# Optimization experiments

Measured on AMD Instinct MI355X. Metric: run time of the kernel, lower is better.

Reference implementation:

```python
import jax, jax.numpy as jnp
import numpy as np

D_MODEL = 1024
N_HEADS = 16
D_K = D_MODEL // N_HEADS


def setup_inputs() -> dict:
    key = jax.random.key(0)
    ks = jax.random.split(key, 10)
    B, L = 2, 2048
    s = 1.0 / np.sqrt(D_MODEL)
    inp = {
        "x": jax.random.normal(ks[0], (B, L, D_MODEL), dtype=jnp.float32),
        "bond_influence": jax.random.uniform(ks[1], (B, L, L), dtype=jnp.float32),
        "Wq": jax.random.uniform(ks[2], (D_MODEL, D_MODEL), jnp.float32, -s, s),
        "bq": jax.random.uniform(ks[3], (D_MODEL,), jnp.float32, -s, s),
        "Wk": jax.random.uniform(ks[4], (D_MODEL, D_MODEL), jnp.float32, -s, s),
        "bk": jax.random.uniform(ks[5], (D_MODEL,), jnp.float32, -s, s),
        "Wv": jax.random.uniform(ks[6], (D_MODEL, D_MODEL), jnp.float32, -s, s),
        "bv": jax.random.uniform(ks[7], (D_MODEL,), jnp.float32, -s, s),
        "Wo": jax.random.uniform(ks[8], (D_MODEL, D_MODEL), jnp.float32, -s, s),
        "bo": jax.random.uniform(ks[9], (D_MODEL,), jnp.float32, -s, s),
    }
    return inp


def reference(x, bond_influence, Wq, bq, Wk, bk, Wv, bv, Wo, bo):
    B, L, _ = x.shape
    # QKV projections -> [B, H, L, d_k]
    def proj(W, b):
        return (x @ W + b).reshape(B, L, N_HEADS, D_K).transpose(0, 2, 1, 3)
    Q = proj(Wq, bq)
    K = proj(Wk, bk)
    V = proj(Wv, bv)
    # scores: [B, H, L, L], scaled then modulated by per-batch bond influence
    scores = jnp.einsum('bhqd,bhkd->bhqk', Q, K) / jnp.sqrt(jnp.float32(D_K))
    scores = scores * bond_influence[:, None, :, :]
    attn = jax.nn.softmax(scores, axis=-1)
    out = jnp.einsum('bhqk,bhkd->bhqd', attn, V)  # [B, H, L, d_k]
    out = out.transpose(0, 2, 1, 3).reshape(B, L, D_MODEL)
    return out @ Wo + bo
```

## Files before the change

kernel.cpp:

```cpp
#include <hip/hip_runtime.h>
#include <stdint.h>

typedef unsigned short u16;
typedef __attribute__((ext_vector_type(8))) short bf16x8;
typedef __attribute__((ext_vector_type(4))) float f32x4;

__device__ __forceinline__ u16 f2bf(float f) {
    union { float f; uint32_t u; } v; v.f = f;
    uint32_t u = v.u + 0x7fffu + ((v.u >> 16) & 1u);
    return (u16)(u >> 16);
}

__device__ __forceinline__ uint32_t cvtpk(float a, float b) {
    uint32_t d;
    asm("v_cvt_pk_bf16_f32 %0, %1, %2" : "=v"(d) : "v"(a), "v"(b));
    return d;
}

__device__ __forceinline__ void gld16(const void* g, void* l) {
    __builtin_amdgcn_global_load_lds((const __attribute__((address_space(1))) void*)g,
                                     (__attribute__((address_space(3))) void*)l,
                                     16, 0, 0);
}

__device__ __forceinline__ void plswap16(uint32_t& a, uint32_t& b) {
    asm volatile("v_permlane16_swap_b32 %0, %1" : "+v"(a), "+v"(b));
}


__global__ void cvt_bf16_kernel(const float* __restrict__ s, u16* __restrict__ d, int n4) {
    int i = blockIdx.x * blockDim.x + threadIdx.x;
    const int stride = gridDim.x * blockDim.x;
    for (; i < n4; i += stride) {
        float4 v = ((const float4*)s)[i];
        ushort4 o;
        o.x = f2bf(v.x); o.y = f2bf(v.y); o.z = f2bf(v.z); o.w = f2bf(v.w);
        ((ushort4*)d)[i] = o;
    }
}

__global__ void transpose4_bf16_kernel(const float* __restrict__ Wq, const float* __restrict__ Wk,
                                       const float* __restrict__ Wv, const float* __restrict__ Wo,
                                       u16* __restrict__ dqkv, u16* __restrict__ dо) {
    __shared__ float tile[32][33];
    const int z = blockIdx.z;
    const float* src = (z == 0) ? Wq : (z == 1) ? Wk : (z == 2) ? Wv : Wo;
    u16* dst = (z < 3) ? (dqkv + (size_t)z * 1024 * 1024) : dо;
    const int tx = threadIdx.x, ty = threadIdx.y;
    const int bx = blockIdx.x * 32, by = blockIdx.y * 32;
#pragma unroll
    for (int i = ty; i < 32; i += 8)
        tile[i][tx] = src[(size_t)(by + i) * 1024 + bx + tx];
    __syncthreads();
#pragma unroll
    for (int i = ty; i < 32; i += 8)
        dst[(size_t)(bx + i) * 1024 + by + tx] = f2bf(tile[tx][i]);
}


template <int EPI>
__global__ __launch_bounds__(256) void gemm128(
    const u16* __restrict__ A, const u16* __restrict__ Bt,
    const float* __restrict__ bias0, const float* __restrict__ bias1,
    const float* __restrict__ bias2,
    u16* __restrict__ o_q, u16* __restrict__ o_k, u16* __restrict__ o_vt,
    float* __restrict__ o_f)
{
    constexpr int K = 1024;
    __shared__ u16 As[128 * 32];
    __shared__ u16 Bs[128 * 32];
    const int t = threadIdx.x;
    const int lane = t & 63, w = t >> 6;
    const int wm = w >> 1, wn = w & 1;
    const int g = lane >> 4, r = lane & 15;
    const int mbase = blockIdx.y * 128, nbase = blockIdx.x * 128;

    const f32x4 zero4 = {0.f, 0.f, 0.f, 0.f};
    f32x4 acc[4][4];
#pragma unroll
    for (int m = 0; m < 4; ++m)
#pragma unroll
        for (int n = 0; n < 4; ++n) acc[m][n] = zero4;

    for (int k0 = 0; k0 < K; k0 += 32) {
#pragma unroll
        for (int i = 0; i < 2; ++i) {
            const int base = i * 256 + (w << 6);
            const int idx = base + lane;
            const int row = idx >> 2, cc = (idx & 3) << 3;
            gld16(A + (size_t)(mbase + row) * K + k0 + cc, (char*)As + base * 16);
            gld16(Bt + (size_t)(nbase + row) * K + k0 + cc, (char*)Bs + base * 16);
        }
        __syncthreads();

        bf16x8 af[4], bfr[4];
#pragma unroll
        for (int m = 0; m < 4; ++m)
            af[m] = *(const bf16x8*)&As[(wm * 64 + m * 16 + r) * 32 + g * 8];
#pragma unroll
        for (int n = 0; n < 4; ++n)
            bfr[n] = *(const bf16x8*)&Bs[(wn * 64 + n * 16 + r) * 32 + g * 8];
        __builtin_amdgcn_s_setprio(1);
#pragma unroll
        for (int m = 0; m < 4; ++m)
#pragma unroll
            for (int n = 0; n < 4; ++n)
                acc[m][n] = __builtin_amdgcn_mfma_f32_16x16x32_bf16(af[m], bfr[n], acc[m][n], 0, 0, 0);
        __builtin_amdgcn_s_setprio(0);
        __syncthreads();
    }

#pragma unroll
    for (int m = 0; m < 4; ++m) {
#pragma unroll
        for (int n = 0; n < 4; ++n) {
            const int c = nbase + wn * 64 + n * 16 + r;
#pragma unroll
            for (int j = 0; j < 4; ++j) {
                const int rr = mbase + wm * 64 + m * 16 + g * 4 + j;
                const float y = acc[m][n][j];
                if (EPI == 0) {
                    const int which = c >> 10, d = c & 1023;
                    const int b = rr >> 11, l = rr & 2047;
                    const int h = d >> 6, dd = d & 63;
                    const size_t bh = (size_t)(b * 16 + h);
                    if (which == 0) {
                        o_q[(bh * 2048 + l) * 64 + dd] = f2bf((y + bias0[d]) * 0.125f);
                    } else if (which == 1) {
                        o_k[(bh * 2048 + l) * 64 + dd] = f2bf(y + bias1[d]);
                    } else {
                        o_vt[(bh * 64 + dd) * 2048 + l] = f2bf(y + bias2[d]);
                    }
                } else {
                    o_f[(size_t)rr * 1024 + c] = y + bias0[c];
                }
            }
        }
    }
}


#define ATTN_STEP(CUR, BD, BDN, PREF)                                                        \
    {                                                                                        \
        if (PREF) {                                                                          \
            const int ktn = kt + 32;                                                         \
            _Pragma("unroll")                                                                \
            for (int i = 0; i < 2; ++i) {                                                    \
                const int idx = i * 128 + t;                                                 \
                const int row = idx >> 3, ch = idx & 7;                                      \
                gld16(kb + kvBase + (size_t)(ktn + row) * 64 + ((ch ^ (row & 7)) << 3),      \
                      (char*)&Ks[CUR ^ 1][0] + idx * 16);                                    \
            }                                                                                \
            _Pragma("unroll")                                                                \
            for (int i = 0; i < 2; ++i) {                                                    \
                const int idx = i * 128 + t;                                                 \
                const int row = idx >> 2, ch = idx & 3;                                      \
                const int chs = ch ^ ((row & 3) ^ ((row >> 2) & 3));                         \
                gld16(vtb + vtBase + (size_t)row * 2048 + ktn + (chs << 3),                  \
                      (char*)&Vs[CUR ^ 1][0] + idx * 16);                                    \
            }                                                                                \
            BDN[0] = *(const float4*)&bondf[bondRowG + ktn];                                 \
            BDN[1] = *(const float4*)&bondf[bondRowG + ktn + 16];                            \
        }                                                                                    \
        bf16x8 k00, k01, k10, k11;                                                           \
        k00 = *(const bf16x8*)((const char*)&Ks[CUR][0] + (r) * 128 + ((g ^ sw) * 16));      \
        k01 = *(const bf16x8*)((const char*)&Ks[CUR][0] + (16 + r) * 128 + ((g ^ sw) * 16)); \
        k10 = *(const bf16x8*)((const char*)&Ks[CUR][0] + (r) * 128 + (((4 + g) ^ sw) * 16)); \
        k11 = *(const bf16x8*)((const char*)&Ks[CUR][0] + (16 + r) * 128 + (((4 + g) ^ sw) * 16)); \
        f32x4 st0, st1;                                                                      \
        __builtin_amdgcn_s_setprio(1);                                                       \
        st0 = __builtin_amdgcn_mfma_f32_16x16x32_bf16(k00, aq0, zero4, 0, 0, 0);             \
        st1 = __builtin_amdgcn_mfma_f32_16x16x32_bf16(k01, aq0, zero4, 0, 0, 0);             \
        st0 = __builtin_amdgcn_mfma_f32_16x16x32_bf16(k10, aq1, st0, 0, 0, 0);               \
        st1 = __builtin_amdgcn_mfma_f32_16x16x32_bf16(k11, aq1, st1, 0, 0, 0);               \
        __builtin_amdgcn_s_setprio(0);                                                       \
        const float p0 = __expf(st0[0] * BD[0].x);                                           \
        const float p1 = __expf(st0[1] * BD[0].y);                                           \
        const float p2 = __expf(st0[2] * BD[0].z);                                           \
        const float p3 = __expf(st0[3] * BD[0].w);                                           \
        const float p4 = __expf(st1[0] * BD[1].x);                                           \
        const float p5 = __expf(st1[1] * BD[1].y);                                           \
        const float p6 = __expf(st1[2] * BD[1].z);                                           \
        const float p7 = __expf(st1[3] * BD[1].w);                                           \
        sm += ((p0 + p1) + (p2 + p3)) + ((p4 + p5) + (p6 + p7));                             \
        uint32_t l0 = cvtpk(p0, p1), h0 = cvtpk(p2, p3);                                     \
        uint32_t l1 = cvtpk(p4, p5), h1 = cvtpk(p6, p7);                                     \
        plswap16(l0, l1);                                                                    \
        plswap16(h0, h1);                                                                    \
        union { uint32_t u[4]; bf16x8 v; } ap_;                                              \
        ap_.u[0] = l0; ap_.u[1] = h0; ap_.u[2] = l1; ap_.u[3] = h1;                          \
        bf16x8 bv0, bv1, bv2, bv3;                                                           \
        bv0 = *(const bf16x8*)((const char*)&Vs[CUR][0] + (r) * 64 + ((pg ^ sv) * 16));      \
        bv1 = *(const bf16x8*)((const char*)&Vs[CUR][0] + (16 + r) * 64 + ((pg ^ sv) * 16)); \
        bv2 = *(const bf16x8*)((const char*)&Vs[CUR][0] + (32 + r) * 64 + ((pg ^ sv) * 16)); \
        bv3 = *(const bf16x8*)((const char*)&Vs[CUR][0] + (48 + r) * 64 + ((pg ^ sv) * 16)); \
        __builtin_amdgcn_s_setprio(1);                                                       \
        o0 = __builtin_amdgcn_mfma_f32_16x16x32_bf16(ap_.v, bv0, o0, 0, 0, 0);               \
        o1 = __builtin_amdgcn_mfma_f32_16x16x32_bf16(ap_.v, bv1, o1, 0, 0, 0);               \
        o2 = __builtin_amdgcn_mfma_f32_16x16x32_bf16(ap_.v, bv2, o2, 0, 0, 0);               \
        o3 = __builtin_amdgcn_mfma_f32_16x16x32_bf16(ap_.v, bv3, o3, 0, 0, 0);               \
        __builtin_amdgcn_s_setprio(0);                                                       \
        __syncthreads();                                                                     \
        kt += 32;                                                                            \
    }

__global__ __launch_bounds__(128, 4) void attn_kernel(
    const u16* __restrict__ qb, const u16* __restrict__ kb,
    const u16* __restrict__ vtb, const float* __restrict__ bondf,
    u16* __restrict__ attnout)
{
    __shared__ u16 Ks[2][32 * 64];
    __shared__ u16 Vs[2][64 * 32];
    const int t = threadIdx.x;
    const int lane = t & 63, w = t >> 6;
    const int g = lane >> 4, r = lane & 15;
    const int sw = r & 7;
    const int sv = (r & 3) ^ ((r >> 2) & 3);
    const int pg = ((g & 1) << 1) | (g >> 1);
    const int flat = blockIdx.x;
    const int wg = (flat & 7) * 256 + (flat >> 3);
    const int bh = wg >> 6, qt = wg & 63;
    const int b = bh >> 4, h = bh & 15;
    const int q0 = qt * 32 + w * 16;
    const size_t kvBase = (size_t)bh * 2048 * 64;
    const size_t vtBase = (size_t)bh * 64 * 2048;
    const size_t bondRowG = ((size_t)b * 2048 + q0 + r) * 2048 + g * 4;

    const bf16x8 aq0 = *(const bf16x8*)&qb[kvBase + (size_t)(q0 + r) * 64 + g * 8];
    const bf16x8 aq1 = *(const bf16x8*)&qb[kvBase + (size_t)(q0 + r) * 64 + 32 + g * 8];

    const f32x4 zero4 = {0.f, 0.f, 0.f, 0.f};
    f32x4 o0 = zero4, o1 = zero4, o2 = zero4, o3 = zero4;
    float sm = 0.f;

#pragma unroll
    for (int i = 0; i < 2; ++i) {
        const int idx = i * 128 + t;
        const int row = idx >> 3, ch = idx & 7;
        gld16(kb + kvBase + (size_t)row * 64 + ((ch ^ (row & 7)) << 3),
              (char*)&Ks[0][0] + idx * 16);
    }
#pragma unroll
    for (int i = 0; i < 2; ++i) {
        const int idx = i * 128 + t;
        const int row = idx >> 2, ch = idx & 3;
        const int chs = ch ^ ((row & 3) ^ ((row >> 2) & 3));
        gld16(vtb + vtBase + (size_t)row * 2048 + (chs << 3),
              (char*)&Vs[0][0] + idx * 16);
    }
    float4 bdA[2], bdB[2];
    bdA[0] = *(const float4*)&bondf[bondRowG];
    bdA[1] = *(const float4*)&bondf[bondRowG + 16];
    __syncthreads();

    int kt = 0;
    for (int s = 0; s < 32; ++s) {
        ATTN_STEP(0, bdA, bdB, true)
        ATTN_STEP(1, bdB, bdA, (s < 31))
    }

    sm += __shfl_xor(sm, 16, 64);
    sm += __shfl_xor(sm, 32, 64);
#pragma unroll
    for (int j = 0; j < 4; ++j) {
        const float inv = 1.f / __shfl(sm, g * 4 + j, 16);
        const size_t orow = ((size_t)b * 2048 + q0 + g * 4 + j) * 1024 + h * 64;
        attnout[orow + r]      = f2bf(o0[j] * inv);
        attnout[orow + 16 + r] = f2bf(o1[j] * inv);
        attnout[orow + 32 + r] = f2bf(o2[j] * inv);
        attnout[orow + 48 + r] = f2bf(o3[j] * inv);
    }
}


extern "C" void kernel_launch(void* const* d_in, const int* in_sizes, int n_in,
                              void* d_out, int out_size, void* d_ws, size_t ws_size,
                              hipStream_t stream) {
    (void)in_sizes; (void)n_in; (void)out_size; (void)ws_size;
    const float* x    = (const float*)d_in[0];
    const float* bond = (const float*)d_in[1];
    const float* Wq   = (const float*)d_in[2];
    const float* bq   = (const float*)d_in[3];
    const float* Wk   = (const float*)d_in[4];
    const float* bk   = (const float*)d_in[5];
    const float* Wv   = (const float*)d_in[6];
    const float* bv   = (const float*)d_in[7];
    const float* Wo   = (const float*)d_in[8];
    const float* bo   = (const float*)d_in[9];
    float* out = (float*)d_out;

    char* ws = (char*)d_ws;
    u16* xb      = (u16*)(ws);
    u16* wqkvt   = (u16*)(ws + 8388608);
    u16* wot     = (u16*)(ws + 14680064);
    u16* qb      = (u16*)(ws + 16777216);
    u16* kb_     = (u16*)(ws + 25165824);
    u16* vtb     = (u16*)(ws + 33554432);
    u16* attnout = (u16*)(ws + 58720256);

    dim3 tb(32, 8);
    transpose4_bf16_kernel<<<dim3(32, 32, 4), tb, 0, stream>>>(Wq, Wk, Wv, Wo, wqkvt, wot);
    cvt_bf16_kernel<<<1024, 256, 0, stream>>>(x, xb, 4194304 / 4);

    gemm128<0><<<dim3(24, 32), 256, 0, stream>>>(xb, wqkvt, bq, bk, bv, qb, kb_, vtb, nullptr);
    attn_kernel<<<dim3(2048), 128, 0, stream>>>(qb, kb_, vtb, bond, attnout);
    gemm128<1><<<dim3(8, 32), 256, 0, stream>>>(attnout, wot, bo, nullptr, nullptr,
                                                nullptr, nullptr, nullptr, out);
}
```

Measured before the change: 188.3 us.

## Use single-wave attention blocks handling 32 query rows with exp2 and vmcnt waits

The attention kernel now runs one 64-lane wave per block covering 32 query rows (two 16-row fragments), so each K/V tile in LDS is reused across twice as many queries and the per-step __syncthreads is replaced by an explicit s_waitcnt vmcnt. The Q scale folds in log2(e) so the softmax uses the raw v_exp_f32 (exp2) instruction instead of __expf. This cuts barrier overhead and LDS/global traffic per query but doubles register use per wave, which may lower occupancy. A scale parameter was also added to the conversion kernel but is set to 1.

```diff
diff --git a/kernel.cpp b/kernel.cpp
--- a/kernel.cpp
+++ b/kernel.cpp
@@ -10,7 +10,11 @@
     uint32_t u = v.u + 0x7fffu + ((v.u >> 16) & 1u);
     return (u16)(u >> 16);
 }
-
+__device__ __forceinline__ float vexp2(float x) {
+    float d;
+    asm("v_exp_f32 %0, %1" : "=v"(d) : "v"(x));
+    return d;
+}
 __device__ __forceinline__ uint32_t cvtpk(float a, float b) {
     uint32_t d;
     asm("v_cvt_pk_bf16_f32 %0, %1, %2" : "=v"(d) : "v"(a), "v"(b));
@@ -28,13 +32,15 @@
 }
 
 
-__global__ void cvt_bf16_kernel(const float* __restrict__ s, u16* __restrict__ d, int n4) {
+__global__ void cvt_bf16_kernel(const float* __restrict__ s, u16* __restrict__ d, int n4,
+                                float scale) {
     int i = blockIdx.x * blockDim.x + threadIdx.x;
     const int stride = gridDim.x * blockDim.x;
     for (; i < n4; i += stride) {
         float4 v = ((const float4*)s)[i];
         ushort4 o;
-        o.x = f2bf(v.x); o.y = f2bf(v.y); o.z = f2bf(v.z); o.w = f2bf(v.w);
+        o.x = f2bf(v.x * scale); o.y = f2bf(v.y * scale);
+        o.z = f2bf(v.z * scale); o.w = f2bf(v.w * scale);
         ((ushort4*)d)[i] = o;
     }
 }
@@ -125,7 +131,7 @@
                     const int h = d >> 6, dd = d & 63;
                     const size_t bh = (size_t)(b * 16 + h);
                     if (which == 0) {
-                        o_q[(bh * 2048 + l) * 64 + dd] = f2bf((y + bias0[d]) * 0.125f);
+                        o_q[(bh * 2048 + l) * 64 + dd] = f2bf((y + bias0[d]) * 0.18033688011112042f);
                     } else if (which == 1) {
                         o_k[(bh * 2048 + l) * 64 + dd] = f2bf(y + bias1[d]);
                     } else {
@@ -140,79 +146,98 @@
 }
 
 
-#define ATTN_STEP(CUR, BD, BDN, PREF)                                                        \
+#define ATTN_STEP(CUR, BD, BDN, PREF, WAITN)                                                 \
     {                                                                                        \
         if (PREF) {                                                                          \
-            const int ktn = kt + 32;                                                         \
-            _Pragma("unroll")                                                                \
-            for (int i = 0; i < 2; ++i) {                                                    \
-                const int idx = i * 128 + t;                                                 \
+            const int kt2 = kt + 32;                                                         \
+            _Pragma("unroll")                                                                \
+            for (int i = 0; i < 4; ++i) {                                                    \
+                const int idx = i * 64 + lane;                                               \
                 const int row = idx >> 3, ch = idx & 7;                                      \
-                gld16(kb + kvBase + (size_t)(ktn + row) * 64 + ((ch ^ (row & 7)) << 3),      \
+                gld16(kb + kvBase + (size_t)(kt2 + row) * 64 + ((ch ^ (row & 7)) << 3),      \
                       (char*)&Ks[CUR ^ 1][0] + idx * 16);                                    \
             }                                                                                \
             _Pragma("unroll")                                                                \
-            for (int i = 0; i < 2; ++i) {                                                    \
-                const int idx = i * 128 + t;                                                 \
+            for (int i = 0; i < 4; ++i) {                                                    \
+                const int idx = i * 64 + lane;                                               \
                 const int row = idx >> 2, ch = idx & 3;                                      \
                 const int chs = ch ^ ((row & 3) ^ ((row >> 2) & 3));                         \
-                gld16(vtb + vtBase + (size_t)row * 2048 + ktn + (chs << 3),                  \
+                gld16(vtb + vtBase + (size_t)row * 2048 + kt2 + (chs << 3),                  \
                       (char*)&Vs[CUR ^ 1][0] + idx * 16);                                    \
             }                                                                                \
-            BDN[0] = *(const float4*)&bondf[bondRowG + ktn];                                 \
-            BDN[1] = *(const float4*)&bondf[bondRowG + ktn + 16];                            \
+            BDN[0] = *(const float4*)&bondf[bondRow0 + kt2 + g * 4];                         \
+            BDN[1] = *(const float4*)&bondf[bondRow0 + kt2 + 16 + g * 4];                    \
+            BDN[2] = *(const float4*)&bondf[bondRow0 + 32768 + kt2 + g * 4];                 \
+            BDN[3] = *(const float4*)&bondf[bondRow0 + 32768 + kt2 + 16 + g * 4];            \
         }                                                                                    \
-        bf16x8 k00, k01, k10, k11;                                                           \
-        k00 = *(const bf16x8*)((const char*)&Ks[CUR][0] + (r) * 128 + ((g ^ sw) * 16));      \
-        k01 = *(const bf16x8*)((const char*)&Ks[CUR][0] + (16 + r) * 128 + ((g ^ sw) * 16)); \
-        k10 = *(const bf16x8*)((const char*)&Ks[CUR][0] + (r) * 128 + (((4 + g) ^ sw) * 16)); \
-        k11 = *(const bf16x8*)((const char*)&Ks[CUR][0] + (16 + r) * 128 + (((4 + g) ^ sw) * 16)); \
-        f32x4 st0, st1;                                                                      \
+        asm volatile("s_waitcnt vmcnt(" #WAITN ")" ::: "memory");                            \
+        __builtin_amdgcn_sched_barrier(0);                                                   \
+                                                \
+        bf16x8 kfr[2][2];                                                                    \
+        _Pragma("unroll")                                                                    \
+        for (int kz = 0; kz < 2; ++kz)                                                       \
+            _Pragma("unroll")                                                                \
+            for (int kf = 0; kf < 2; ++kf)                                                   \
+                kfr[kz][kf] = *(const bf16x8*)((const char*)&Ks[CUR][0] +                    \
+                                (kf * 16 + r) * 128 + (((kz * 4 + g) ^ sw) * 16));           \
+        f32x4 st[2][2];                                                                      \
         __builtin_amdgcn_s_setprio(1);                                                       \
-        st0 = __builtin_amdgcn_mfma_f32_16x16x32_bf16(k00, aq0, zero4, 0, 0, 0);             \
-        st1 = __builtin_amdgcn_mfma_f32_16x16x32_bf16(k01, aq0, zero4, 0, 0, 0);             \
-        st0 = __builtin_amdgcn_mfma_f32_16x16x32_bf16(k10, aq1, st0, 0, 0, 0);               \
-        st1 = __builtin_amdgcn_mfma_f32_16x16x32_bf16(k11, aq1, st1, 0, 0, 0);               \
+        _Pragma("unroll")                                                                    \
+        for (int qf = 0; qf < 2; ++qf)                                                       \
+            _Pragma("unroll")                                                                \
+            for (int kf = 0; kf < 2; ++kf) {                                                 \
+                st[qf][kf] = __builtin_amdgcn_mfma_f32_16x16x32_bf16(                        \
+                    kfr[0][kf], aq[qf][0], zero4, 0, 0, 0);                                  \
+                st[qf][kf] = __builtin_amdgcn_mfma_f32_16x16x32_bf16(                        \
+                    kfr[1][kf], aq[qf][1], st[qf][kf], 0, 0, 0);                             \
+            }                                                                                \
         __builtin_amdgcn_s_setprio(0);                                                       \
-        const float p0 = __expf(st0[0] * BD[0].x);                                           \
-        const float p1 = __expf(st0[1] * BD[0].y);                                           \
-        const float p2 = __expf(st0[2] * BD[0].z);                                           \
-        const float p3 = __expf(st0[3] * BD[0].w);                                           \
-        const float p4 = __expf(st1[0] * BD[1].x);                                           \
-        const float p5 = __expf(st1[1] * BD[1].y);                                           \
-        const float p6 = __expf(st1[2] * BD[1].z);                                           \
-        const float p7 = __expf(st1[3] * BD[1].w);                                           \
-        sm += ((p0 + p1) + (p2 + p3)) + ((p4 + p5) + (p6 + p7));                             \
-        uint32_t l0 = cvtpk(p0, p1), h0 = cvtpk(p2, p3);                                     \
-        uint32_t l1 = cvtpk(p4, p5), h1 = cvtpk(p6, p7);                                     \
-        plswap16(l0, l1);                                                                    \
-        plswap16(h0, h1);                                                                    \
-        union { uint32_t u[4]; bf16x8 v; } ap_;                                              \
-        ap_.u[0] = l0; ap_.u[1] = h0; ap_.u[2] = l1; ap_.u[3] = h1;                          \
-        bf16x8 bv0, bv1, bv2, bv3;                                                           \
-        bv0 = *(const bf16x8*)((const char*)&Vs[CUR][0] + (r) * 64 + ((pg ^ sv) * 16));      \
-        bv1 = *(const bf16x8*)((const char*)&Vs[CUR][0] + (16 + r) * 64 + ((pg ^ sv) * 16)); \
-        bv2 = *(const bf16x8*)((const char*)&Vs[CUR][0] + (32 + r) * 64 + ((pg ^ sv) * 16)); \
-        bv3 = *(const bf16x8*)((const char*)&Vs[CUR][0] + (48 + r) * 64 + ((pg ^ sv) * 16)); \
+                                                \
+        bf16x8 ap[2];                                                                        \
+        _Pragma("unroll")                                                                    \
+        for (int qf = 0; qf < 2; ++qf) {                                                     \
+            const float p0 = vexp2(st[qf][0][0] * BD[2 * qf].x);                             \
+            const float p1 = vexp2(st[qf][0][1] * BD[2 * qf].y);                             \
+            const float p2 = vexp2(st[qf][0][2] * BD[2 * qf].z);                             \
+            const float p3 = vexp2(st[qf][0][3] * BD[2 * qf].w);                             \
+            const float p4 = vexp2(st[qf][1][0] * BD[2 * qf + 1].x);                         \
+            const float p5 = vexp2(st[qf][1][1] * BD[2 * qf + 1].y);                         \
+            const float p6 = vexp2(st[qf][1][2] * BD[2 * qf + 1].z);                         \
+            const float p7 = vexp2(st[qf][1][3] * BD[2 * qf + 1].w);                         \
+            sm[qf] += ((p0 + p1) + (p2 + p3)) + ((p4 + p5) + (p6 + p7));                     \
+            uint32_t l0 = cvtpk(p0, p1), h0 = cvtpk(p2, p3);                                 \
+            uint32_t l1 = cvtpk(p4, p5), h1 = cvtpk(p6, p7);                                 \
+            plswap16(l0, l1);                                                                \
+            plswap16(h0, h1);                                                                \
+            union { uint32_t u[4]; bf16x8 v; } a_;                                           \
+            a_.u[0] = l0; a_.u[1] = h0; a_.u[2] = l1; a_.u[3] = h1;                          \
+            ap[qf] = a_.v;                                                                   \
+        }                                                                                    \
+                                              \
+        bf16x8 bv_[4];                                                                       \
+        _Pragma("unroll")                                                                    \
+        for (int nf = 0; nf < 4; ++nf)                                                       \
+            bv_[nf] = *(const bf16x8*)((const char*)&Vs[CUR][0] +                            \
+                        (nf * 16 + r) * 64 + ((pg ^ sv) << 4));                              \
         __builtin_amdgcn_s_setprio(1);                                                       \
-        o0 = __builtin_amdgcn_mfma_f32_16x16x32_bf16(ap_.v, bv0, o0, 0, 0, 0);               \
-        o1 = __builtin_amdgcn_mfma_f32_16x16x32_bf16(ap_.v, bv1, o1, 0, 0, 0);               \
-        o2 = __builtin_amdgcn_mfma_f32_16x16x32_bf16(ap_.v, bv2, o2, 0, 0, 0);               \
-        o3 = __builtin_amdgcn_mfma_f32_16x16x32_bf16(ap_.v, bv3, o3, 0, 0, 0);               \
+        _Pragma("unroll")                                                                    \
+        for (int qf = 0; qf < 2; ++qf)                                                       \
+            _Pragma("unroll")                                                                \
+            for (int nf = 0; nf < 4; ++nf)                                                   \
+                o[qf][nf] = __builtin_amdgcn_mfma_f32_16x16x32_bf16(                         \
+                    ap[qf], bv_[nf], o[qf][nf], 0, 0, 0);                                    \
         __builtin_amdgcn_s_setprio(0);                                                       \
-        __syncthreads();                                                                     \
         kt += 32;                                                                            \
     }
 
-__global__ __launch_bounds__(128, 4) void attn_kernel(
+__global__ __launch_bounds__(64) void attn_kernel(
     const u16* __restrict__ qb, const u16* __restrict__ kb,
     const u16* __restrict__ vtb, const float* __restrict__ bondf,
     u16* __restrict__ attnout)
 {
     __shared__ u16 Ks[2][32 * 64];
     __shared__ u16 Vs[2][64 * 32];
-    const int t = threadIdx.x;
-    const int lane = t & 63, w = t >> 6;
+    const int lane = threadIdx.x & 63;
     const int g = lane >> 4, r = lane & 15;
     const int sw = r & 7;
     const int sv = (r & 3) ^ ((r >> 2) & 3);
@@ -221,55 +246,70 @@
     const int wg = (flat & 7) * 256 + (flat >> 3);
     const int bh = wg >> 6, qt = wg & 63;
     const int b = bh >> 4, h = bh & 15;
-    const int q0 = qt * 32 + w * 16;
+    const int q0 = qt * 32;
     const size_t kvBase = (size_t)bh * 2048 * 64;
     const size_t vtBase = (size_t)bh * 64 * 2048;
-    const size_t bondRowG = ((size_t)b * 2048 + q0 + r) * 2048 + g * 4;
-
-    const bf16x8 aq0 = *(const bf16x8*)&qb[kvBase + (size_t)(q0 + r) * 64 + g * 8];
-    const bf16x8 aq1 = *(const bf16x8*)&qb[kvBase + (size_t)(q0 + r) * 64 + 32 + g * 8];
+    const size_t bondRow0 = ((size_t)b * 2048 + q0 + r) * 2048;
+
+    bf16x8 aq[2][2];
+#pragma unroll
+    for (int qf = 0; qf < 2; ++qf)
+#pragma unroll
+        for (int kz = 0; kz < 2; ++kz)
+            aq[qf][kz] = *(const bf16x8*)&qb[kvBase + (size_t)(q0 + qf * 16 + r) * 64 + kz * 32 + g * 8];
 
     const f32x4 zero4 = {0.f, 0.f, 0.f, 0.f};
-    f32x4 o0 = zero4, o1 = zero4, o2 = zero4, o3 = zero4;
-    float sm = 0.f;
-
-#pragma unroll
-    for (int i = 0; i < 2; ++i) {
-        const int idx = i * 128 + t;
+    f32x4 o[2][4];
+#pragma unroll
+    for (int qf = 0; qf < 2; ++qf)
+#pragma unroll
+        for (int nf = 0; nf < 4; ++nf) o[qf][nf] = zero4;
+    float sm[2] = {0.f, 0.f};
+
+#pragma unroll
+    for (int i = 0; i < 4; ++i) {
+        const int idx = i * 64 + lane;
         const int row = idx >> 3, ch = idx & 7;
         gld16(kb + kvBase + (size_t)row * 64 + ((ch ^ (row & 7)) << 3),
               (char*)&Ks[0][0] + idx * 16);
     }
 #pragma unroll
-    for (int i = 0; i < 2; ++i) {
-        const int idx = i * 128 + t;
+    for (int i = 0; i < 4; ++i) {
+        const int idx = i * 64 + lane;
         const int row = idx >> 2, ch = idx & 3;
         const int chs = ch ^ ((row & 3) ^ ((row >> 2) & 3));
         gld16(vtb + vtBase + (size_t)row * 2048 + (chs << 3),
               (char*)&Vs[0][0] + idx * 16);
     }
-    float4 bdA[2], bdB[2];
-    bdA[0] = *(const float4*)&bondf[bondRowG];
-    bdA[1] = *(const float4*)&bondf[bondRowG + 16];
-    __syncthreads();
+    float4 bdA[4], bdB[4];
+    bdA[0] = *(const float4*)&bondf[bondRow0 + g * 4];
+    bdA[1] = *(const float4*)&bondf[bondRow0 + 16 + g * 4];
+    bdA[2] = *(const float4*)&bondf[bondRow0 + 32768 + g * 4];
+    bdA[3] = *(const float4*)&bondf[bondRow0 + 32768 + 16 + g * 4];
 
     int kt = 0;
-    for (int s = 0; s < 32; ++s) {
-        ATTN_STEP(0, bdA, bdB, true)
-        ATTN_STEP(1, bdB, bdA, (s < 31))
-    }
-
-    sm += __shfl_xor(sm, 16, 64);
-    sm += __shfl_xor(sm, 32, 64);
-#pragma unroll
-    for (int j = 0; j < 4; ++j) {
-        const float inv = 1.f / __shfl(sm, g * 4 + j, 16);
-        const size_t orow = ((size_t)b * 2048 + q0 + g * 4 + j) * 1024 + h * 64;
-        attnout[orow + r]      = f2bf(o0[j] * inv);
-        attnout[orow + 16 + r] = f2bf(o1[j] * inv);
-        attnout[orow + 32 + r] = f2bf(o2[j] * inv);
-        attnout[orow + 48 + r] = f2bf(o3[j] * inv);
-    }
+    for (int s = 0; s < 31; ++s) {
+        ATTN_STEP(0, bdA, bdB, 1, 16)
+        ATTN_STEP(1, bdB, bdA, 1, 16)
+    }
+    ATTN_STEP(0, bdA, bdB, 1, 16)
+    ATTN_STEP(1, bdB, bdA, 0, 4)
+
+#pragma unroll
+    for (int qf = 0; qf < 2; ++qf) {
+        sm[qf] += __shfl_xor(sm[qf], 16, 64);
+        sm[qf] += __shfl_xor(sm[qf], 32, 64);
+    }
+#pragma unroll
+    for (int qf = 0; qf < 2; ++qf)
+#pragma unroll
+        for (int j = 0; j < 4; ++j) {
+            const float inv = 1.f / __shfl(sm[qf], g * 4 + j, 16);
+            const size_t orow = ((size_t)b * 2048 + q0 + qf * 16 + g * 4 + j) * 1024 + h * 64;
+#pragma unroll
+            for (int nf = 0; nf < 4; ++nf)
+                attnout[orow + nf * 16 + r] = f2bf(o[qf][nf][j] * inv);
+        }
 }
 
 
@@ -300,10 +340,10 @@
 
     dim3 tb(32, 8);
     transpose4_bf16_kernel<<<dim3(32, 32, 4), tb, 0, stream>>>(Wq, Wk, Wv, Wo, wqkvt, wot);
-    cvt_bf16_kernel<<<1024, 256, 0, stream>>>(x, xb, 4194304 / 4);
+    cvt_bf16_kernel<<<1024, 256, 0, stream>>>(x, xb, 4194304 / 4, 1.0f);
 
     gemm128<0><<<dim3(24, 32), 256, 0, stream>>>(xb, wqkvt, bq, bk, bv, qb, kb_, vtb, nullptr);
-    attn_kernel<<<dim3(2048), 128, 0, stream>>>(qb, kb_, vtb, bond, attnout);
+    attn_kernel<<<dim3(2048), 64, 0, stream>>>(qb, kb_, vtb, bond, attnout);
     gemm128<1><<<dim3(8, 32), 256, 0, stream>>>(attnout, wot, bo, nullptr, nullptr,
                                                 nullptr, nullptr, nullptr, out);
 }
```

Result: no change. 185.5 us (-1.5%).
